# Kernel tuning notes

Hardware: AMD Instinct MI355X
Metric: run time of the kernel (lower is better)

## Reference

```python
import itertools
import jax, jax.numpy as jnp
import numpy as np

B, S, H = 1, 2048, 1024
NH, KVH, HD = 16, 8, 64
E, TOPK, I = 8, 2, 3584
EPS = 1e-6
THETA = 1000000.0
COMBS = np.array(list(itertools.combinations(range(E), TOPK)), dtype=np.int32)  # [28,2]


def setup_inputs() -> dict:
    key = jax.random.key(0)
    ks = jax.random.split(key, 12)
    s = 0.02
    return {
        "hidden_states": jax.random.normal(ks[0], (B, S, H), jnp.float32),
        "ln1_w": jnp.ones((H,), jnp.float32),
        "ln2_w": jnp.ones((H,), jnp.float32),
        "wq": jax.random.normal(ks[1], (NH * HD, H), jnp.float32) * s,
        "wk": jax.random.normal(ks[2], (KVH * HD, H), jnp.float32) * s,
        "wv": jax.random.normal(ks[3], (KVH * HD, H), jnp.float32) * s,
        "wo": jax.random.normal(ks[4], (H, NH * HD), jnp.float32) * s,
        "gate_w": jax.random.normal(ks[5], (E, H), jnp.float32) * s,
        "w1": jax.random.normal(ks[6], (E, I, H), jnp.float32) * s,
        "w2": jax.random.normal(ks[7], (E, H, I), jnp.float32) * s,
        "w3": jax.random.normal(ks[8], (E, I, H), jnp.float32) * s,
    }


def _rmsnorm(x, w):
    v = x.astype(jnp.float32)
    v = v * jax.lax.rsqrt(jnp.mean(v * v, axis=-1, keepdims=True) + EPS)
    return (w * v).astype(x.dtype)


def _rotate_half(x):
    h = x.shape[-1] // 2
    return jnp.concatenate([-x[..., h:], x[..., :h]], axis=-1)


def reference(hidden_states, ln1_w, ln2_w, wq, wk, wv, wo, gate_w, w1, w2, w3):
    residual = hidden_states
    x = _rmsnorm(hidden_states, ln1_w)

    # --- Mixtral attention (GQA + RoPE, causal) ---
    q = (x @ wq.T).reshape(B, S, NH, HD).transpose(0, 2, 1, 3)   # [B,NH,S,HD]
    k = (x @ wk.T).reshape(B, S, KVH, HD).transpose(0, 2, 1, 3)  # [B,KVH,S,HD]
    v = (x @ wv.T).reshape(B, S, KVH, HD).transpose(0, 2, 1, 3)

    pos = jnp.arange(S, dtype=jnp.float32)
    inv_freq = 1.0 / (THETA ** (jnp.arange(0, HD, 2, dtype=jnp.float32) / HD))
    freqs = pos[:, None] * inv_freq[None, :]               # [S,HD/2]
    emb = jnp.concatenate([freqs, freqs], axis=-1)          # [S,HD]
    cos, sin = jnp.cos(emb)[None, None], jnp.sin(emb)[None, None]
    q = q * cos + _rotate_half(q) * sin
    k = k * cos + _rotate_half(k) * sin

    rep = NH // KVH
    k = jnp.repeat(k, rep, axis=1)
    v = jnp.repeat(v, rep, axis=1)

    scores = jnp.einsum("bhsd,bhtd->bhst", q, k) / jnp.sqrt(jnp.float32(HD))
    causal = jnp.tril(jnp.ones((S, S), dtype=bool))
    scores = jnp.where(causal[None, None], scores, jnp.finfo(jnp.float32).min)
    attn = jax.nn.softmax(scores.astype(jnp.float32), axis=-1).astype(q.dtype)
    ctx = jnp.einsum("bhst,bhtd->bhsd", attn, v)
    ctx = ctx.transpose(0, 2, 1, 3).reshape(B, S, NH * HD)
    hidden_states = residual + ctx @ wo.T

    # --- MoE block (combination routing, no experts_used mask) ---
    residual = hidden_states
    x = _rmsnorm(hidden_states, ln2_w).reshape(-1, H)       # [N,H], N=B*S
    N = x.shape[0]
    router_logits = x @ gate_w.T                            # [N,E]
    rw = jax.nn.softmax(router_logits.astype(jnp.float32), axis=-1)

    combs = jnp.asarray(COMBS)                              # [28,2]
    comb_scores = jnp.take(rw, combs, axis=1).sum(-1)       # [N,28]
    sel = jnp.argmax(comb_scores, axis=-1)                  # [N]
    selected_experts = combs[sel]                           # [N,TOPK]
    w = jnp.take_along_axis(rw, selected_experts, axis=1)   # [N,TOPK]
    w = (w / w.sum(-1, keepdims=True)).astype(x.dtype)

    # per-token per-expert combine weights (0 if not selected)
    wm = jnp.zeros((N, E), x.dtype).at[jnp.arange(N)[:, None], selected_experts].set(w)

    # dense evaluation of all experts, combined by sparse weights
    h1 = jax.nn.silu(jnp.einsum("nh,eih->nei", x, w1))
    h3 = jnp.einsum("nh,eih->nei", x, w3)
    out_e = jnp.einsum("nei,ehi->neh", h1 * h3, w2)          # [N,E,H]
    moe_out = jnp.einsum("neh,ne->nh", out_e, wm)

    hidden_states = residual + moe_out.reshape(B, S, H)
    return hidden_states
```

## Files before the change

### kernel.cpp

```cpp
#include <hip/hip_runtime.h>
#include <hip/hip_bf16.h>
#include <math.h>

constexpr int S_ = 2048, H_ = 1024, NH_ = 16, KVH_ = 8, HD_ = 64;
constexpr int E_ = 8, I_ = 3584;
constexpr int KSLC = 4;
constexpr float EPS_ = 1e-6f;
constexpr float THETA_ = 1000000.0f;

#define SDIV(a,b) (((a)+(b)-1)/(b))

typedef __attribute__((ext_vector_type(8))) short bf16x8;
typedef __attribute__((ext_vector_type(4))) float f32x4;

__device__ inline unsigned pkbf(float a, float b) {
    unsigned r;
    asm("v_cvt_pk_bf16_f32 %0, %1, %2" : "=v"(r) : "v"(a), "v"(b));
    return r;
}
__device__ inline unsigned short f2bf(float f) {
    unsigned u = __float_as_uint(f);
    u += 0x7FFF + ((u >> 16) & 1);
    return (unsigned short)(u >> 16);
}
__device__ inline float bf2f(unsigned short v) {
    return __uint_as_float((unsigned)v << 16);
}

__device__ inline void gload16u(const void* gsrc, char* ldsArr, int uoff) {
    int off = __builtin_amdgcn_readfirstlane(uoff);
    __builtin_amdgcn_global_load_lds(
        (__attribute__((address_space(1))) void*)(gsrc),
        (__attribute__((address_space(3))) void*)(ldsArr + off), 16, 0, 0);
}
__device__ inline void vmdrain() {
    asm volatile("s_waitcnt vmcnt(0)" ::: "memory");
}

template<bool WB>
__device__ inline int4 loadW16(const void* W, size_t elemOff) {
    if constexpr (WB) {
        return *(const int4*)((const unsigned short*)W + elemOff);
    } else {
        const float* s = (const float*)W + elemOff;
        float4 f0 = *(const float4*)s, f1 = *(const float4*)(s + 4);
        return make_int4(pkbf(f0.x, f0.y), pkbf(f0.z, f0.w),
                         pkbf(f1.x, f1.y), pkbf(f1.z, f1.w));
    }
}

__global__ __launch_bounds__(256) void conv_bf16(const float* __restrict__ in,
                                                 unsigned short* __restrict__ out, long n8)
{
    long i = (long)blockIdx.x * 256 + threadIdx.x;
    long stride = (long)gridDim.x * 256;
    for (; i < n8; i += stride) {
        const float* s = in + i * 8;
        float4 f0 = *(const float4*)s, f1 = *(const float4*)(s + 4);
        *(int4*)(out + i * 8) = make_int4(pkbf(f0.x, f0.y), pkbf(f0.z, f0.w),
                                          pkbf(f1.x, f1.y), pkbf(f1.z, f1.w));
    }
}

__global__ __launch_bounds__(256) void rmsnorm_k(const float* __restrict__ x,
                                                 const float* __restrict__ w,
                                                 float* __restrict__ out,
                                                 unsigned short* __restrict__ outb)
{
    int row = blockIdx.x;
    int tid = threadIdx.x;
    const float* xr = x + (size_t)row * H_;
    float4 v = *(const float4*)&xr[tid * 4];
    float ss = v.x*v.x + v.y*v.y + v.z*v.z + v.w*v.w;
#pragma unroll
    for (int off = 32; off > 0; off >>= 1) ss += __shfl_xor(ss, off);
    __shared__ float red[4];
    if ((tid & 63) == 0) red[tid >> 6] = ss;
    __syncthreads();
    float tot = red[0] + red[1] + red[2] + red[3];
    float r = rsqrtf(tot / (float)H_ + EPS_);
    float4 wv = *(const float4*)&w[tid * 4];
    float4 o;
    o.x = v.x * r * wv.x; o.y = v.y * r * wv.y;
    o.z = v.z * r * wv.z; o.w = v.w * r * wv.w;
    *(float4*)&out[(size_t)row * H_ + tid * 4] = o;
    if (outb) {
        uint2 pk = make_uint2(pkbf(o.x, o.y), pkbf(o.z, o.w));
        *(uint2*)&outb[(size_t)row * H_ + tid * 4] = pk;
    }
}

template<bool WB>
__global__ __launch_bounds__(256) void dense_mfma(const float* __restrict__ A,
                                                  const void* __restrict__ Bw,
                                                  const float* __restrict__ Res,
                                                  float* __restrict__ C,
                                                  int M, int N, int K)
{
    __shared__ char As[16384], Bs[16384];
    int tid = threadIdx.x;
    int m0 = blockIdx.y * 128, n0 = blockIdx.x * 128;
    int lane = tid & 63, w = tid >> 6, wm = w >> 1, wn = w & 1;
    int lm = lane & 15, lk = lane >> 4;

    int4 rA[4], rB[4];
    auto loadAll = [&](int kb) {
#pragma unroll
        for (int it = 0; it < 4; ++it) {
            int g = tid + it * 256, row = g >> 3, kg = g & 7;
            const float* s = A + (size_t)(m0 + row) * K + kb + kg * 8;
            float4 f0 = *(const float4*)s, f1 = *(const float4*)(s + 4);
            rA[it] = make_int4(pkbf(f0.x, f0.y), pkbf(f0.z, f0.w),
                               pkbf(f1.x, f1.y), pkbf(f1.z, f1.w));
            rB[it] = loadW16<WB>(Bw, (size_t)(n0 + row) * K + kb + kg * 8);
        }
    };
    auto writeAll = [&]() {
#pragma unroll
        for (int it = 0; it < 4; ++it) {
            int g = tid + it * 256, row = g >> 3, kg = g & 7;
            int byte = row * 128 + ((kg * 16) ^ ((row & 7) << 4));
            *(int4*)(As + byte) = rA[it];
            *(int4*)(Bs + byte) = rB[it];
        }
    };

    f32x4 z = {0.f, 0.f, 0.f, 0.f};
    f32x4 acc[4][4];
#pragma unroll
    for (int mf = 0; mf < 4; ++mf)
#pragma unroll
        for (int nf = 0; nf < 4; ++nf) acc[mf][nf] = z;

    loadAll(0);
    for (int kt = 0; kt < K / 64; ++kt) {
        __syncthreads();
        writeAll();
        __syncthreads();
        if (kt + 1 < K / 64) loadAll((kt + 1) * 64);
#pragma unroll
        for (int ks = 0; ks < 2; ++ks) {
            bf16x8 af[4];
#pragma unroll
            for (int mf = 0; mf < 4; ++mf) {
                int row = wm * 64 + mf * 16 + lm;
                af[mf] = *(const bf16x8*)(As + row * 128 + ((ks * 64 + lk * 16) ^ ((row & 7) << 4)));
            }
#pragma unroll
            for (int nf = 0; nf < 4; ++nf) {
                int brow = wn * 64 + nf * 16 + lm;
                bf16x8 bf = *(const bf16x8*)(Bs + brow * 128 + ((ks * 64 + lk * 16) ^ ((brow & 7) << 4)));
#pragma unroll
                for (int mf = 0; mf < 4; ++mf)
                    acc[mf][nf] = __builtin_amdgcn_mfma_f32_16x16x32_bf16(af[mf], bf, acc[mf][nf], 0, 0, 0);
            }
        }
    }

#pragma unroll
    for (int mf = 0; mf < 4; ++mf)
#pragma unroll
        for (int nf = 0; nf < 4; ++nf) {
            int col = n0 + wn * 64 + nf * 16 + lm;
#pragma unroll
            for (int j = 0; j < 4; ++j) {
                int row = m0 + wm * 64 + mf * 16 + lk * 4 + j;
                float r = Res ? Res[(size_t)row * N + col] : 0.0f;
                C[(size_t)row * N + col] = acc[mf][nf][j] + r;
            }
        }
}

__global__ __launch_bounds__(256) void rope_conv(const float* __restrict__ q,
                                                 const float* __restrict__ k,
                                                 unsigned short* __restrict__ qbf,
                                                 unsigned short* __restrict__ kbf)
{
    int idx = blockIdx.x * 256 + threadIdx.x;
    const int totq = S_ * NH_ * 32;
    const int tot = totq + S_ * KVH_ * 32;
    if (idx >= tot) return;
    const float* base; unsigned short* obase; int s, di; float sc;
    if (idx < totq) {
        s = idx / (NH_ * 32); int r = idx % (NH_ * 32);
        size_t o = ((size_t)s * NH_ + (r >> 5)) * HD_;
        base = q + o; obase = qbf + o; di = r & 31; sc = 0.125f;
    } else {
        int j2 = idx - totq;
        s = j2 / (KVH_ * 32); int r = j2 % (KVH_ * 32);
        size_t o = ((size_t)s * KVH_ + (r >> 5)) * HD_;
        base = k + o; obase = kbf + o; di = r & 31; sc = 1.0f;
    }
    float invf = powf(THETA_, -(2.0f * di) / (float)HD_);
    float ang = (float)s * invf;
    float c = cosf(ang), sn = sinf(ang);
    float x0 = base[di], x1 = base[di + 32];
    obase[di]      = f2bf((x0 * c - x1 * sn) * sc);
    obase[di + 32] = f2bf((x1 * c + x0 * sn) * sc);
}

__global__ __launch_bounds__(256) void v_trans(const float* __restrict__ v,
                                               unsigned short* __restrict__ vtb)
{
    int t0 = blockIdx.x * 64, kvh = blockIdx.y;
    __shared__ unsigned short T[64][64];
    int tid = threadIdx.x;
    int k = tid >> 2, d0 = (tid & 3) * 16;
    const float* src = v + ((size_t)(t0 + k) * KVH_ + kvh) * HD_ + d0;
#pragma unroll
    for (int x = 0; x < 4; ++x) {
        float4 f = *(const float4*)(src + x * 4);
        T[k][d0 + x*4 + 0] = f2bf(f.x);
        T[k][d0 + x*4 + 1] = f2bf(f.y);
        T[k][d0 + x*4 + 2] = f2bf(f.z);
        T[k][d0 + x*4 + 3] = f2bf(f.w);
    }
    __syncthreads();
    int d = tid >> 2, s0 = (tid & 3) * 16;
    unsigned short tmp[16] __attribute__((aligned(16)));
#pragma unroll
    for (int x = 0; x < 16; ++x) {
        int s = s0 + x;
        int key = 16 * (s & 3) + (s >> 2);
        tmp[x] = T[key][d];
    }
    unsigned short* dst = vtb + ((size_t)kvh * HD_ + d) * S_ + t0 + s0;
    *(int4*)(dst)     = *(int4*)(tmp);
    *(int4*)(dst + 8) = *(int4*)(tmp + 8);
}

__global__ __launch_bounds__(256) void attn_mfma(const unsigned short* __restrict__ qbf,
                                                 const unsigned short* __restrict__ kbf,
                                                 const unsigned short* __restrict__ vtb,
                                                 float* __restrict__ ctx)
{
    __shared__ char Ps[4 * 2048];
    int pair = blockIdx.x, h = blockIdx.y, z = blockIdx.z;
    int qb = z ? (31 - pair) : pair;
    int q0 = qb * 64;
    int kvh = h >> 1;
    int tid = threadIdx.x;
    int w = tid >> 6, lane = tid & 63;
    int lm = lane & 15, lk = lane >> 4;
    char* myP = Ps + w * 2048;

    bf16x8 qf[2];
    const unsigned short* qrow = qbf + ((size_t)(q0 + w * 16 + lm) * NH_ + h) * HD_;
#pragma unroll
    for (int ks = 0; ks < 2; ++ks)
        qf[ks] = *(const bf16x8*)(qrow + ks * 32 + lk * 8);

    float m_[4], l_[4];
    f32x4 o_[4];
#pragma unroll
    for (int j = 0; j < 4; ++j) { m_[j] = -1e30f; l_[j] = 0.f; }
    f32x4 zf = {0.f, 0.f, 0.f, 0.f};
#pragma unroll
    for (int nd = 0; nd < 4; ++nd) o_[nd] = zf;

    for (int t0 = 0; t0 <= q0; t0 += 64) {
        f32x4 s[4];
#pragma unroll
        for (int nf = 0; nf < 4; ++nf) {
            const unsigned short* krow = kbf + ((size_t)(t0 + nf * 16 + lm) * KVH_ + kvh) * HD_;
            bf16x8 k0 = *(const bf16x8*)(krow + lk * 8);
            bf16x8 k1 = *(const bf16x8*)(krow + 32 + lk * 8);
            f32x4 acc = zf;
            acc = __builtin_amdgcn_mfma_f32_16x16x32_bf16(qf[0], k0, acc, 0, 0, 0);
            acc = __builtin_amdgcn_mfma_f32_16x16x32_bf16(qf[1], k1, acc, 0, 0, 0);
            s[nf] = acc;
        }
        if (t0 == q0) {
#pragma unroll
            for (int nf = 0; nf < 4; ++nf)
#pragma unroll
                for (int j = 0; j < 4; ++j) {
                    int key = nf * 16 + lm, qq = w * 16 + lk * 4 + j;
                    if (key > qq) s[nf][j] = -1e30f;
                }
        }
        float p_[4][4];
#pragma unroll
        for (int j = 0; j < 4; ++j) {
            float mx = fmaxf(fmaxf(s[0][j], s[1][j]), fmaxf(s[2][j], s[3][j]));
#pragma unroll
            for (int off = 8; off > 0; off >>= 1) mx = fmaxf(mx, __shfl_xor(mx, off));
            float nm = fmaxf(m_[j], mx);
            float rs = __expf(m_[j] - nm);
            float sum = 0.f;
#pragma unroll
            for (int nf = 0; nf < 4; ++nf) {
                float pv = __expf(s[nf][j] - nm);
                p_[nf][j] = pv; sum += pv;
            }
#pragma unroll
            for (int off = 8; off > 0; off >>= 1) sum += __shfl_xor(sum, off);
            l_[j] = l_[j] * rs + sum;
            m_[j] = nm;
#pragma unroll
            for (int nd = 0; nd < 4; ++nd) o_[nd][j] *= rs;
        }
#pragma unroll
        for (int j = 0; j < 4; ++j) {
            int r = lk * 4 + j;
            unsigned lo = pkbf(p_[0][j], p_[1][j]);
            unsigned hi = pkbf(p_[2][j], p_[3][j]);
            int byte = (lm * 8) ^ ((r & 7) << 4);
            *(uint2*)(myP + r * 128 + byte) = make_uint2(lo, hi);
        }
#pragma unroll
        for (int ks = 0; ks < 2; ++ks) {
            int byte = (ks * 64 + lk * 16) ^ ((lm & 7) << 4);
            bf16x8 pA = *(const bf16x8*)(myP + lm * 128 + byte);
#pragma unroll
            for (int nd = 0; nd < 4; ++nd) {
                const unsigned short* vrow = vtb + ((size_t)kvh * HD_ + nd * 16 + lm) * S_ + t0 + ks * 32 + lk * 8;
                bf16x8 vB = *(const bf16x8*)vrow;
                o_[nd] = __builtin_amdgcn_mfma_f32_16x16x32_bf16(pA, vB, o_[nd], 0, 0, 0);
            }
        }
    }
#pragma unroll
    for (int nd = 0; nd < 4; ++nd)
#pragma unroll
        for (int j = 0; j < 4; ++j) {
            int r = lk * 4 + j;
            ctx[((size_t)(q0 + w * 16 + r) * NH_ + h) * HD_ + nd * 16 + lm] = o_[nd][j] / l_[j];
        }
}

__global__ __launch_bounds__(64) void router_k(const float* __restrict__ x2,
                                               const float* __restrict__ gw,
                                               int* __restrict__ cnt,
                                               int* __restrict__ elist,
                                               int* __restrict__ eslot,
                                               float* __restrict__ wslot)
{
    int n = blockIdx.x, lane = threadIdx.x;
    float part[E_];
#pragma unroll
    for (int e = 0; e < E_; ++e) part[e] = 0.f;
    const float* xr = x2 + (size_t)n * H_;
    for (int j = lane; j < H_; j += 64) {
        float xv = xr[j];
#pragma unroll
        for (int e = 0; e < E_; ++e) part[e] = fmaf(xv, gw[e * H_ + j], part[e]);
    }
#pragma unroll
    for (int e = 0; e < E_; ++e)
#pragma unroll
        for (int off = 32; off > 0; off >>= 1) part[e] += __shfl_xor(part[e], off);
    if (lane == 0) {
        float mx = part[0];
#pragma unroll
        for (int e = 1; e < E_; ++e) mx = fmaxf(mx, part[e]);
        float rw[E_]; float ssum = 0.f;
#pragma unroll
        for (int e = 0; e < E_; ++e) { rw[e] = expf(part[e] - mx); ssum += rw[e]; }
#pragma unroll
        for (int e = 0; e < E_; ++e) rw[e] /= ssum;
        float best = -1.f; int ba = 0, bb = 1;
        for (int a = 0; a < E_; ++a)
            for (int b = a + 1; b < E_; ++b) {
                float scv = rw[a] + rw[b];
                if (scv > best) { best = scv; ba = a; bb = b; }
            }
        float wa = rw[ba], wb = rw[bb], wsum = wa + wb;
        wa /= wsum; wb /= wsum;
        int p = atomicAdd(&cnt[ba], 1);
        elist[ba * S_ + p] = n; eslot[ba * S_ + p] = 2 * n;
        p = atomicAdd(&cnt[bb], 1);
        elist[bb * S_ + p] = n; eslot[bb * S_ + p] = 2 * n + 1;
        wslot[2 * n] = wa; wslot[2 * n + 1] = wb;
    }
}

__global__ __launch_bounds__(256) void moe_up_g(const unsigned short* __restrict__ x2b,
                                                const unsigned short* __restrict__ w1b,
                                                const unsigned short* __restrict__ w3b,
                                                const int* __restrict__ cnt,
                                                const int* __restrict__ elist,
                                                const int* __restrict__ eslot,
                                                unsigned short* __restrict__ hbuf)
{
    int e = blockIdx.z;
    int c = cnt[e];
    int p0 = blockIdx.y * 128;
    if (p0 >= c) return;
    int i0 = blockIdx.x * 64;
    int tid = threadIdx.x;

    __shared__ char As[16384], B1s[8192], B3s[8192];
    __shared__ int rowtokS[128], rowslotS[128];
    if (tid < 128) {
        int p = min(p0 + tid, c - 1);
        rowtokS[tid]  = elist[e * S_ + p];
        rowslotS[tid] = eslot[e * S_ + p];
    }
    __syncthreads();

    int lane = tid & 63, w = tid >> 6, wm = w >> 1, wn = w & 1;
    int lm = lane & 15, lk = lane >> 4;
    int wb16 = (tid & ~63) * 16;
    size_t wbase = (size_t)e * I_ * H_;

    f32x4 z = {0.f, 0.f, 0.f, 0.f};
    f32x4 acc1[4][2], acc3[4][2];
#pragma unroll
    for (int mf = 0; mf < 4; ++mf)
#pragma unroll
        for (int nf = 0; nf < 2; ++nf) { acc1[mf][nf] = z; acc3[mf][nf] = z; }

    for (int kt = 0; kt < H_ / 64; ++kt) {
        int kb = kt * 64;
#pragma unroll
        for (int it = 0; it < 4; ++it) {
            int g = tid + it * 256, row = g >> 3, kg = g & 7;
            int kgs = kg ^ (row & 7);
            gload16u(x2b + (size_t)rowtokS[row] * H_ + kb + kgs * 8, As, wb16 + it * 4096);
        }
#pragma unroll
        for (int it = 0; it < 2; ++it) {
            int g = tid + it * 256, row = g >> 3, kg = g & 7;
            int kgs = kg ^ (row & 7);
            size_t off = wbase + (size_t)(i0 + row) * H_ + kb + kgs * 8;
            gload16u(w1b + off, B1s, wb16 + it * 4096);
            gload16u(w3b + off, B3s, wb16 + it * 4096);
        }
        vmdrain();
        __syncthreads();
#pragma unroll
        for (int ks = 0; ks < 2; ++ks) {
            bf16x8 af[4];
#pragma unroll
            for (int mf = 0; mf < 4; ++mf) {
                int row = wm * 64 + mf * 16 + lm;
                af[mf] = *(const bf16x8*)(As + row * 128 + ((ks * 64 + lk * 16) ^ ((row & 7) << 4)));
            }
#pragma unroll
            for (int nf = 0; nf < 2; ++nf) {
                int brow = wn * 32 + nf * 16 + lm;
                int bby = brow * 128 + ((ks * 64 + lk * 16) ^ ((brow & 7) << 4));
                bf16x8 b1 = *(const bf16x8*)(B1s + bby);
                bf16x8 b3 = *(const bf16x8*)(B3s + bby);
#pragma unroll
                for (int mf = 0; mf < 4; ++mf) {
                    acc1[mf][nf] = __builtin_amdgcn_mfma_f32_16x16x32_bf16(af[mf], b1, acc1[mf][nf], 0, 0, 0);
                    acc3[mf][nf] = __builtin_amdgcn_mfma_f32_16x16x32_bf16(af[mf], b3, acc3[mf][nf], 0, 0, 0);
                }
            }
        }
        __syncthreads();
    }

#pragma unroll
    for (int mf = 0; mf < 4; ++mf)
#pragma unroll
        for (int nf = 0; nf < 2; ++nf) {
            int coli = i0 + wn * 32 + nf * 16 + lm;
#pragma unroll
            for (int j = 0; j < 4; ++j) {
                int rloc = wm * 64 + mf * 16 + lk * 4 + j;
                if (p0 + rloc < c) {
                    float h1 = acc1[mf][nf][j];
                    float val = h1 / (1.f + __expf(-h1)) * acc3[mf][nf][j];
                    hbuf[(size_t)rowslotS[rloc] * I_ + coli] = f2bf(val);
                }
            }
        }
}

__global__ __launch_bounds__(256) void moe_dn_g(const unsigned short* __restrict__ hbuf,
                                                const unsigned short* __restrict__ w2b,
                                                const int* __restrict__ cnt,
                                                const int* __restrict__ eslot,
                                                unsigned short* __restrict__ dbuf)
{
    int e = blockIdx.z >> 2;
    int slice = blockIdx.z & 3;
    int c = cnt[e];
    int p0 = blockIdx.y * 128;
    if (p0 >= c) return;
    int h0 = blockIdx.x * 128;
    int tid = threadIdx.x;
    const int kb0 = slice * (I_ / KSLC);

    __shared__ char As[16384], Bs[16384];
    __shared__ int rowslotS[128];
    if (tid < 128) rowslotS[tid] = eslot[e * S_ + min(p0 + tid, c - 1)];
    __syncthreads();

    int lane = tid & 63, w = tid >> 6, wm = w >> 1, wn = w & 1;
    int lm = lane & 15, lk = lane >> 4;
    int wb16 = (tid & ~63) * 16;
    size_t wbase = (size_t)e * H_ * I_;

    f32x4 z = {0.f, 0.f, 0.f, 0.f};
    f32x4 acc[4][4];
#pragma unroll
    for (int mf = 0; mf < 4; ++mf)
#pragma unroll
        for (int nf = 0; nf < 4; ++nf) acc[mf][nf] = z;

    const int NKT = (I_ / KSLC) / 64;
    for (int kt = 0; kt < NKT; ++kt) {
        int kb = kb0 + kt * 64;
#pragma unroll
        for (int it = 0; it < 4; ++it) {
            int g = tid + it * 256, row = g >> 3, kg = g & 7;
            int kgs = kg ^ (row & 7);
            gload16u(hbuf + (size_t)rowslotS[row] * I_ + kb + kgs * 8, As, wb16 + it * 4096);
            gload16u(w2b + wbase + (size_t)(h0 + row) * I_ + kb + kgs * 8, Bs, wb16 + it * 4096);
        }
        vmdrain();
        __syncthreads();
#pragma unroll
        for (int ks = 0; ks < 2; ++ks) {
            bf16x8 af[4];
#pragma unroll
            for (int mf = 0; mf < 4; ++mf) {
                int row = wm * 64 + mf * 16 + lm;
                af[mf] = *(const bf16x8*)(As + row * 128 + ((ks * 64 + lk * 16) ^ ((row & 7) << 4)));
            }
#pragma unroll
            for (int nf = 0; nf < 4; ++nf) {
                int brow = wn * 64 + nf * 16 + lm;
                bf16x8 bf = *(const bf16x8*)(Bs + brow * 128 + ((ks * 64 + lk * 16) ^ ((brow & 7) << 4)));
#pragma unroll
                for (int mf = 0; mf < 4; ++mf)
                    acc[mf][nf] = __builtin_amdgcn_mfma_f32_16x16x32_bf16(af[mf], bf, acc[mf][nf], 0, 0, 0);
            }
        }
        __syncthreads();
    }

    unsigned short* dslice = dbuf + (size_t)slice * S_ * 2 * H_;
#pragma unroll
    for (int mf = 0; mf < 4; ++mf)
#pragma unroll
        for (int nf = 0; nf < 4; ++nf) {
            int colh = h0 + wn * 64 + nf * 16 + lm;
#pragma unroll
            for (int j = 0; j < 4; ++j) {
                int rloc = wm * 64 + mf * 16 + lk * 4 + j;
                if (p0 + rloc < c)
                    dslice[(size_t)rowslotS[rloc] * H_ + colh] = f2bf(acc[mf][nf][j]);
            }
        }
}

template<bool WB>
__global__ __launch_bounds__(256) void moe_up_mfma(const float* __restrict__ x2,
                                                   const void* __restrict__ w1,
                                                   const void* __restrict__ w3,
                                                   const int* __restrict__ cnt,
                                                   const int* __restrict__ elist,
                                                   const int* __restrict__ eslot,
                                                   unsigned short* __restrict__ hbuf)
{
    int e = blockIdx.z;
    int c = cnt[e];
    int p0 = blockIdx.y * 128;
    if (p0 >= c) return;
    int i0 = blockIdx.x * 64;
    int tid = threadIdx.x;

    __shared__ char As[16384], B1s[8192], B3s[8192];
    __shared__ int rowtokS[128], rowslotS[128];
    if (tid < 128) {
        int p = min(p0 + tid, c - 1);
        rowtokS[tid]  = elist[e * S_ + p];
        rowslotS[tid] = eslot[e * S_ + p];
    }
    __syncthreads();

    int lane = tid & 63, w = tid >> 6, wm = w >> 1, wn = w & 1;
    int lm = lane & 15, lk = lane >> 4;
    size_t wbase = (size_t)e * I_ * H_;

    int4 rA[4], rB1[2], rB3[2];
    auto loadAll = [&](int kb) {
#pragma unroll
        for (int it = 0; it < 4; ++it) {
            int g = tid + it * 256, row = g >> 3, kg = g & 7;
            const float* s = x2 + (size_t)rowtokS[row] * H_ + kb + kg * 8;
            float4 f0 = *(const float4*)s, f1 = *(const float4*)(s + 4);
            rA[it] = make_int4(pkbf(f0.x, f0.y), pkbf(f0.z, f0.w),
                               pkbf(f1.x, f1.y), pkbf(f1.z, f1.w));
        }
#pragma unroll
        for (int it = 0; it < 2; ++it) {
            int g = tid + it * 256, row = g >> 3, kg = g & 7;
            size_t off = wbase + (size_t)(i0 + row) * H_ + kb + kg * 8;
            rB1[it] = loadW16<WB>(w1, off);
            rB3[it] = loadW16<WB>(w3, off);
        }
    };
    auto writeAll = [&]() {
#pragma unroll
        for (int it = 0; it < 4; ++it) {
            int g = tid + it * 256, row = g >> 3, kg = g & 7;
            int byte = row * 128 + ((kg * 16) ^ ((row & 7) << 4));
            *(int4*)(As + byte) = rA[it];
        }
#pragma unroll
        for (int it = 0; it < 2; ++it) {
            int g = tid + it * 256, row = g >> 3, kg = g & 7;
            int byte = row * 128 + ((kg * 16) ^ ((row & 7) << 4));
            *(int4*)(B1s + byte) = rB1[it];
            *(int4*)(B3s + byte) = rB3[it];
        }
    };

    f32x4 z = {0.f, 0.f, 0.f, 0.f};
    f32x4 acc1[4][2], acc3[4][2];
#pragma unroll
    for (int mf = 0; mf < 4; ++mf)
#pragma unroll
        for (int nf = 0; nf < 2; ++nf) { acc1[mf][nf] = z; acc3[mf][nf] = z; }

    loadAll(0);
    for (int kt = 0; kt < H_ / 64; ++kt) {
        __syncthreads();
        writeAll();
        __syncthreads();
        if (kt + 1 < H_ / 64) loadAll((kt + 1) * 64);
#pragma unroll
        for (int ks = 0; ks < 2; ++ks) {
            bf16x8 af[4];
#pragma unroll
            for (int mf = 0; mf < 4; ++mf) {
                int row = wm * 64 + mf * 16 + lm;
                af[mf] = *(const bf16x8*)(As + row * 128 + ((ks * 64 + lk * 16) ^ ((row & 7) << 4)));
            }
#pragma unroll
            for (int nf = 0; nf < 2; ++nf) {
                int brow = wn * 32 + nf * 16 + lm;
                int bby = brow * 128 + ((ks * 64 + lk * 16) ^ ((brow & 7) << 4));
                bf16x8 b1 = *(const bf16x8*)(B1s + bby);
                bf16x8 b3 = *(const bf16x8*)(B3s + bby);
#pragma unroll
                for (int mf = 0; mf < 4; ++mf) {
                    acc1[mf][nf] = __builtin_amdgcn_mfma_f32_16x16x32_bf16(af[mf], b1, acc1[mf][nf], 0, 0, 0);
                    acc3[mf][nf] = __builtin_amdgcn_mfma_f32_16x16x32_bf16(af[mf], b3, acc3[mf][nf], 0, 0, 0);
                }
            }
        }
    }

#pragma unroll
    for (int mf = 0; mf < 4; ++mf)
#pragma unroll
        for (int nf = 0; nf < 2; ++nf) {
            int coli = i0 + wn * 32 + nf * 16 + lm;
#pragma unroll
            for (int j = 0; j < 4; ++j) {
                int rloc = wm * 64 + mf * 16 + lk * 4 + j;
                if (p0 + rloc < c) {
                    float h1 = acc1[mf][nf][j];
                    float val = h1 / (1.f + __expf(-h1)) * acc3[mf][nf][j];
                    hbuf[(size_t)rowslotS[rloc] * I_ + coli] = f2bf(val);
                }
            }
        }
}

template<bool WB>
__global__ __launch_bounds__(256) void moe_dn_mfma(const unsigned short* __restrict__ hbuf,
                                                   const void* __restrict__ w2,
                                                   const int* __restrict__ cnt,
                                                   const int* __restrict__ eslot,
                                                   unsigned short* __restrict__ dbuf)
{
    int e = blockIdx.z >> 2;
    int slice = blockIdx.z & 3;
    int c = cnt[e];
    int p0 = blockIdx.y * 128;
    if (p0 >= c) return;
    int h0 = blockIdx.x * 128;
    int tid = threadIdx.x;
    const int kb0 = slice * (I_ / KSLC);

    __shared__ char As[16384], Bs[16384];
    __shared__ int rowslotS[128];
    if (tid < 128) rowslotS[tid] = eslot[e * S_ + min(p0 + tid, c - 1)];
    __syncthreads();

    int lane = tid & 63, w = tid >> 6, wm = w >> 1, wn = w & 1;
    int lm = lane & 15, lk = lane >> 4;
    size_t wbase = (size_t)e * H_ * I_;

    int4 rA[4], rB[4];
    auto loadAll = [&](int kb) {
#pragma unroll
        for (int it = 0; it < 4; ++it) {
            int g = tid + it * 256, row = g >> 3, kg = g & 7;
            rA[it] = *(const int4*)(hbuf + (size_t)rowslotS[row] * I_ + kb + kg * 8);
            rB[it] = loadW16<WB>(w2, wbase + (size_t)(h0 + row) * I_ + kb + kg * 8);
        }
    };
    auto writeAll = [&]() {
#pragma unroll
        for (int it = 0; it < 4; ++it) {
            int g = tid + it * 256, row = g >> 3, kg = g & 7;
            int byte = row * 128 + ((kg * 16) ^ ((row & 7) << 4));
            *(int4*)(As + byte) = rA[it];
            *(int4*)(Bs + byte) = rB[it];
        }
    };

    f32x4 z = {0.f, 0.f, 0.f, 0.f};
    f32x4 acc[4][4];
#pragma unroll
    for (int mf = 0; mf < 4; ++mf)
#pragma unroll
        for (int nf = 0; nf < 4; ++nf) acc[mf][nf] = z;

    loadAll(kb0);
    const int NKT = (I_ / KSLC) / 64;
    for (int kt = 0; kt < NKT; ++kt) {
        __syncthreads();
        writeAll();
        __syncthreads();
        if (kt + 1 < NKT) loadAll(kb0 + (kt + 1) * 64);
#pragma unroll
        for (int ks = 0; ks < 2; ++ks) {
            bf16x8 af[4];
#pragma unroll
            for (int mf = 0; mf < 4; ++mf) {
                int row = wm * 64 + mf * 16 + lm;
                af[mf] = *(const bf16x8*)(As + row * 128 + ((ks * 64 + lk * 16) ^ ((row & 7) << 4)));
            }
#pragma unroll
            for (int nf = 0; nf < 4; ++nf) {
                int brow = wn * 64 + nf * 16 + lm;
                bf16x8 bf = *(const bf16x8*)(Bs + brow * 128 + ((ks * 64 + lk * 16) ^ ((brow & 7) << 4)));
#pragma unroll
                for (int mf = 0; mf < 4; ++mf)
                    acc[mf][nf] = __builtin_amdgcn_mfma_f32_16x16x32_bf16(af[mf], bf, acc[mf][nf], 0, 0, 0);
            }
        }
    }

    unsigned short* dslice = dbuf + (size_t)slice * S_ * 2 * H_;
#pragma unroll
    for (int mf = 0; mf < 4; ++mf)
#pragma unroll
        for (int nf = 0; nf < 4; ++nf) {
            int colh = h0 + wn * 64 + nf * 16 + lm;
#pragma unroll
            for (int j = 0; j < 4; ++j) {
                int rloc = wm * 64 + mf * 16 + lk * 4 + j;
                if (p0 + rloc < c)
                    dslice[(size_t)rowslotS[rloc] * H_ + colh] = f2bf(acc[mf][nf][j]);
            }
        }
}

__global__ __launch_bounds__(256) void combine_k(const float* __restrict__ hid2,
                                                 const unsigned short* __restrict__ dbuf,
                                                 const float* __restrict__ wslot,
                                                 float* __restrict__ out)
{
    int idx = blockIdx.x * 256 + threadIdx.x;
    if (idx >= S_ * H_) return;
    int n = idx >> 10;
    int hcol = idx & (H_ - 1);
    float s0 = 0.f, s1 = 0.f;
#pragma unroll
    for (int sl = 0; sl < KSLC; ++sl) {
        const unsigned short* base = dbuf + (size_t)sl * S_ * 2 * H_;
        s0 += bf2f(base[(size_t)(2 * n)     * H_ + hcol]);
        s1 += bf2f(base[(size_t)(2 * n + 1) * H_ + hcol]);
    }
    out[idx] = hid2[idx] + wslot[2 * n] * s0 + wslot[2 * n + 1] * s1;
}

extern "C" void kernel_launch(void* const* d_in, const int* in_sizes, int n_in,
                              void* d_out, int out_size, void* d_ws, size_t ws_size,
                              hipStream_t stream)
{
    const float* hidden = (const float*)d_in[0];
    const float* ln1    = (const float*)d_in[1];
    const float* ln2    = (const float*)d_in[2];
    const float* wq     = (const float*)d_in[3];
    const float* wk     = (const float*)d_in[4];
    const float* wv     = (const float*)d_in[5];
    const float* wo     = (const float*)d_in[6];
    const float* gw     = (const float*)d_in[7];
    const float* w1     = (const float*)d_in[8];
    const float* w2     = (const float*)d_in[9];
    const float* w3     = (const float*)d_in[10];
    float* out = (float*)d_out;

    char* p = (char*)d_ws;
    auto alignp = [&]() { p = (char*)(((uintptr_t)p + 255) & ~(uintptr_t)255); };
    auto alloc_f = [&](size_t n) { alignp(); float* r = (float*)p; p += n * 4; return r; };
    auto alloc_h = [&](size_t n) { alignp(); unsigned short* r = (unsigned short*)p; p += n * 2; return r; };
    auto alloc_i = [&](size_t n) { alignp(); int* r = (int*)p; p += n * 4; return r; };

    float* xb   = alloc_f((size_t)S_ * H_);
    float* q    = alloc_f((size_t)S_ * NH_ * HD_);
    float* kb   = alloc_f((size_t)S_ * KVH_ * HD_);
    float* vb   = alloc_f((size_t)S_ * KVH_ * HD_);
    float* hid2 = alloc_f((size_t)S_ * H_);
    float* x2   = alloc_f((size_t)S_ * H_);
    unsigned short* x2b  = alloc_h((size_t)S_ * H_);
    unsigned short* hbuf = alloc_h((size_t)S_ * 2 * I_);
    unsigned short* dbuf = alloc_h((size_t)KSLC * S_ * 2 * H_);
    float* wslot= alloc_f((size_t)S_ * 2);
    unsigned short* qbf = alloc_h((size_t)S_ * NH_ * HD_);
    unsigned short* kbf = alloc_h((size_t)S_ * KVH_ * HD_);
    unsigned short* vtb = alloc_h((size_t)KVH_ * HD_ * S_);
    int* cnt   = alloc_i(E_);
    int* elist = alloc_i((size_t)E_ * S_);
    int* eslot = alloc_i((size_t)E_ * S_);
    float* ctx = xb;

    size_t used = (size_t)(p - (char*)d_ws);
    const size_t nW = (size_t)E_ * I_ * H_;
    size_t wbf_bytes = (3 * nW + (size_t)(NH_*HD_ + 2*KVH_*HD_ + H_) * H_) * 2 + 4096;
    bool WB = ws_size > used && (ws_size - used) >= wbf_bytes;

    unsigned short *w1b = nullptr, *w3b = nullptr, *w2b = nullptr;
    unsigned short *wqb = nullptr, *wkb = nullptr, *wvb = nullptr, *wob = nullptr;
    if (WB) {
        w1b = alloc_h(nW); w3b = alloc_h(nW); w2b = alloc_h(nW);
        wqb = alloc_h((size_t)NH_ * HD_ * H_);
        wkb = alloc_h((size_t)KVH_ * HD_ * H_);
        wvb = alloc_h((size_t)KVH_ * HD_ * H_);
        wob = alloc_h((size_t)H_ * NH_ * HD_);
    }

    hipMemsetAsync(cnt, 0, E_ * sizeof(int), stream);

    if (WB) {
        conv_bf16<<<2048, 256, 0, stream>>>(w1, w1b, (long)(nW / 8));
        conv_bf16<<<2048, 256, 0, stream>>>(w3, w3b, (long)(nW / 8));
        conv_bf16<<<2048, 256, 0, stream>>>(w2, w2b, (long)(nW / 8));
        conv_bf16<<<512, 256, 0, stream>>>(wq, wqb, (long)((size_t)NH_*HD_*H_ / 8));
        conv_bf16<<<512, 256, 0, stream>>>(wk, wkb, (long)((size_t)KVH_*HD_*H_ / 8));
        conv_bf16<<<512, 256, 0, stream>>>(wv, wvb, (long)((size_t)KVH_*HD_*H_ / 8));
        conv_bf16<<<512, 256, 0, stream>>>(wo, wob, (long)((size_t)H_*NH_*HD_ / 8));
    }

    rmsnorm_k<<<S_, 256, 0, stream>>>(hidden, ln1, xb, nullptr);

    if (WB) {
        dense_mfma<true><<<dim3(8, 16),  256, 0, stream>>>(xb, wqb, nullptr, q,  S_, NH_ * HD_, H_);
        dense_mfma<true><<<dim3(4, 16),  256, 0, stream>>>(xb, wkb, nullptr, kb, S_, KVH_ * HD_, H_);
        dense_mfma<true><<<dim3(4, 16),  256, 0, stream>>>(xb, wvb, nullptr, vb, S_, KVH_ * HD_, H_);
    } else {
        dense_mfma<false><<<dim3(8, 16), 256, 0, stream>>>(xb, wq, nullptr, q,  S_, NH_ * HD_, H_);
        dense_mfma<false><<<dim3(4, 16), 256, 0, stream>>>(xb, wk, nullptr, kb, S_, KVH_ * HD_, H_);
        dense_mfma<false><<<dim3(4, 16), 256, 0, stream>>>(xb, wv, nullptr, vb, S_, KVH_ * HD_, H_);
    }
    {
        int tot = S_ * (NH_ + KVH_) * 32;
        rope_conv<<<SDIV(tot, 256), 256, 0, stream>>>(q, kb, qbf, kbf);
    }
    v_trans<<<dim3(S_ / 64, KVH_), 256, 0, stream>>>(vb, vtb);
    attn_mfma<<<dim3(16, NH_, 2), 256, 0, stream>>>(qbf, kbf, vtb, ctx);

    if (WB)
        dense_mfma<true><<<dim3(8, 16),  256, 0, stream>>>(ctx, wob, hidden, hid2, S_, H_, NH_ * HD_);
    else
        dense_mfma<false><<<dim3(8, 16), 256, 0, stream>>>(ctx, wo, hidden, hid2, S_, H_, NH_ * HD_);

    rmsnorm_k<<<S_, 256, 0, stream>>>(hid2, ln2, x2, x2b);
    router_k<<<S_, 64, 0, stream>>>(x2, gw, cnt, elist, eslot, wslot);

    if (WB) {
        moe_up_g<<<dim3(I_ / 64, S_ / 128, E_), 256, 0, stream>>>(x2b, w1b, w3b, cnt, elist, eslot, hbuf);
        moe_dn_g<<<dim3(H_ / 128, S_ / 128, E_ * KSLC), 256, 0, stream>>>(hbuf, w2b, cnt, eslot, dbuf);
    } else {
        moe_up_mfma<false><<<dim3(I_ / 64, S_ / 128, E_), 256, 0, stream>>>(x2, w1, w3, cnt, elist, eslot, hbuf);
        moe_dn_mfma<false><<<dim3(H_ / 128, S_ / 128, E_ * KSLC), 256, 0, stream>>>(hbuf, w2, cnt, eslot, dbuf);
    }
    combine_k<<<SDIV(S_ * H_, 256), 256, 0, stream>>>(hid2, dbuf, wslot, out);
}
```

Baseline: 539.1 us.

## Fuse QKV projections into one bf16 GEMM with bf16 activations

Concatenates the Q, K and V weights into one bf16 matrix and runs a single bf16-input GEMM (new dense_g kernel, 128x64 tiles, 512 blocks) that writes bf16 QKV output. RoPE and V-transpose kernels now read that bf16 buffer, and attention also writes a bf16 context copy that feeds the output projection through the same bf16 GEMM. This removes fp32 activation loads and conversions and two kernel launches, and gives more blocks per GEMM for better occupancy. In exchange attention writes an extra bf16 context buffer, and q/k are rounded to bf16 before RoPE, which may add small numerical error.

```diff
diff --git a/kernel.cpp b/kernel.cpp
--- a/kernel.cpp
+++ b/kernel.cpp
@@ -90,6 +90,82 @@
     }
 }
 
+template<bool OUTF32>
+__global__ __launch_bounds__(256) void dense_g(const unsigned short* __restrict__ A,
+                                               const unsigned short* __restrict__ B,
+                                               const float* __restrict__ Res,
+                                               void* __restrict__ C,
+                                               int K, int ldC)
+{
+    int m0 = blockIdx.y * 128, n0 = blockIdx.x * 64;
+    int tid = threadIdx.x;
+    __shared__ char As[16384], Bs[8192];
+    int lane = tid & 63, w = tid >> 6, wm = w >> 1, wn = w & 1;
+    int lm = lane & 15, lk = lane >> 4;
+    int wb16 = (tid & ~63) * 16;
+
+    f32x4 z = {0.f, 0.f, 0.f, 0.f};
+    f32x4 acc[4][2];
+#pragma unroll
+    for (int mf = 0; mf < 4; ++mf)
+#pragma unroll
+        for (int nf = 0; nf < 2; ++nf) acc[mf][nf] = z;
+
+    for (int kt = 0; kt < K / 64; ++kt) {
+        int kb = kt * 64;
+#pragma unroll
+        for (int it = 0; it < 4; ++it) {
+            int g = tid + it * 256, row = g >> 3, kg = g & 7;
+            int kgs = kg ^ (row & 7);
+            gload16u(A + (size_t)(m0 + row) * K + kb + kgs * 8, As, wb16 + it * 4096);
+        }
+#pragma unroll
+        for (int it = 0; it < 2; ++it) {
+            int g = tid + it * 256, row = g >> 3, kg = g & 7;
+            int kgs = kg ^ (row & 7);
+            gload16u(B + (size_t)(n0 + row) * K + kb + kgs * 8, Bs, wb16 + it * 4096);
+        }
+        vmdrain();
+        __syncthreads();
+#pragma unroll
+        for (int ks = 0; ks < 2; ++ks) {
+            bf16x8 af[4];
+#pragma unroll
+            for (int mf = 0; mf < 4; ++mf) {
+                int row = wm * 64 + mf * 16 + lm;
+                af[mf] = *(const bf16x8*)(As + row * 128 + ((ks * 64 + lk * 16) ^ ((row & 7) << 4)));
+            }
+#pragma unroll
+            for (int nf = 0; nf < 2; ++nf) {
+                int brow = wn * 32 + nf * 16 + lm;
+                bf16x8 bf = *(const bf16x8*)(Bs + brow * 128 + ((ks * 64 + lk * 16) ^ ((brow & 7) << 4)));
+#pragma unroll
+                for (int mf = 0; mf < 4; ++mf)
+                    acc[mf][nf] = __builtin_amdgcn_mfma_f32_16x16x32_bf16(af[mf], bf, acc[mf][nf], 0, 0, 0);
+            }
+        }
+        __syncthreads();
+    }
+
+#pragma unroll
+    for (int mf = 0; mf < 4; ++mf)
+#pragma unroll
+        for (int nf = 0; nf < 2; ++nf) {
+            int col = n0 + wn * 32 + nf * 16 + lm;
+#pragma unroll
+            for (int j = 0; j < 4; ++j) {
+                int row = m0 + wm * 64 + mf * 16 + lk * 4 + j;
+                float v = acc[mf][nf][j];
+                if constexpr (OUTF32) {
+                    float r = Res ? Res[(size_t)row * ldC + col] : 0.0f;
+                    ((float*)C)[(size_t)row * ldC + col] = v + r;
+                } else {
+                    ((unsigned short*)C)[(size_t)row * ldC + col] = f2bf(v);
+                }
+            }
+        }
+}
+
 template<bool WB>
 __global__ __launch_bounds__(256) void dense_mfma(const float* __restrict__ A,
                                                   const void* __restrict__ Bw,
@@ -169,6 +245,59 @@
                 C[(size_t)row * N + col] = acc[mf][nf][j] + r;
             }
         }
+}
+
+__global__ __launch_bounds__(256) void rope_conv_b(const unsigned short* __restrict__ qkvb,
+                                                   unsigned short* __restrict__ qbf,
+                                                   unsigned short* __restrict__ kbf)
+{
+    int idx = blockIdx.x * 256 + threadIdx.x;
+    const int totq = S_ * NH_ * 32;
+    const int tot = totq + S_ * KVH_ * 32;
+    if (idx >= tot) return;
+    const unsigned short* src; unsigned short* dst; int s, di; float sc;
+    if (idx < totq) {
+        s = idx / (NH_ * 32); int r = idx % (NH_ * 32); int h = r >> 5;
+        src = qkvb + (size_t)s * 2048 + h * 64;
+        dst = qbf + ((size_t)s * NH_ + h) * HD_;
+        di = r & 31; sc = 0.125f;
+    } else {
+        int j2 = idx - totq;
+        s = j2 / (KVH_ * 32); int r = j2 % (KVH_ * 32); int kvh = r >> 5;
+        src = qkvb + (size_t)s * 2048 + 1024 + kvh * 64;
+        dst = kbf + ((size_t)s * KVH_ + kvh) * HD_;
+        di = r & 31; sc = 1.0f;
+    }
+    float invf = powf(THETA_, -(2.0f * di) / (float)HD_);
+    float ang = (float)s * invf;
+    float c = cosf(ang), sn = sinf(ang);
+    float x0 = bf2f(src[di]), x1 = bf2f(src[di + 32]);
+    dst[di]      = f2bf((x0 * c - x1 * sn) * sc);
+    dst[di + 32] = f2bf((x1 * c + x0 * sn) * sc);
+}
+
+__global__ __launch_bounds__(256) void v_trans_b(const unsigned short* __restrict__ qkvb,
+                                                 unsigned short* __restrict__ vtb)
+{
+    int t0 = blockIdx.x * 64, kvh = blockIdx.y;
+    __shared__ unsigned short T[64][64];
+    int tid = threadIdx.x;
+    int k = tid >> 2, d0 = (tid & 3) * 16;
+    const unsigned short* src = qkvb + (size_t)(t0 + k) * 2048 + 1536 + kvh * 64 + d0;
+    *(int4*)&T[k][d0]     = *(const int4*)(src);
+    *(int4*)&T[k][d0 + 8] = *(const int4*)(src + 8);
+    __syncthreads();
+    int d = tid >> 2, s0 = (tid & 3) * 16;
+    unsigned short tmp[16] __attribute__((aligned(16)));
+#pragma unroll
+    for (int x = 0; x < 16; ++x) {
+        int s = s0 + x;
+        int key = 16 * (s & 3) + (s >> 2);
+        tmp[x] = T[key][d];
+    }
+    unsigned short* dst = vtb + ((size_t)kvh * HD_ + d) * S_ + t0 + s0;
+    *(int4*)(dst)     = *(int4*)(tmp);
+    *(int4*)(dst + 8) = *(int4*)(tmp + 8);
 }
 
 __global__ __launch_bounds__(256) void rope_conv(const float* __restrict__ q,
@@ -232,7 +361,8 @@
 __global__ __launch_bounds__(256) void attn_mfma(const unsigned short* __restrict__ qbf,
                                                  const unsigned short* __restrict__ kbf,
                                                  const unsigned short* __restrict__ vtb,
-                                                 float* __restrict__ ctx)
+                                                 float* __restrict__ ctx,
+                                                 unsigned short* __restrict__ ctxb)
 {
     __shared__ char Ps[4 * 2048];
     int pair = blockIdx.x, h = blockIdx.y, z = blockIdx.z;
@@ -325,7 +455,10 @@
 #pragma unroll
         for (int j = 0; j < 4; ++j) {
             int r = lk * 4 + j;
-            ctx[((size_t)(q0 + w * 16 + r) * NH_ + h) * HD_ + nd * 16 + lm] = o_[nd][j] / l_[j];
+            float val = o_[nd][j] / l_[j];
+            size_t oidx = ((size_t)(q0 + w * 16 + r) * NH_ + h) * HD_ + nd * 16 + lm;
+            ctx[oidx] = val;
+            ctxb[oidx] = f2bf(val);
         }
 }
 
@@ -800,12 +933,15 @@
     auto alloc_i = [&](size_t n) { alignp(); int* r = (int*)p; p += n * 4; return r; };
 
     float* xb   = alloc_f((size_t)S_ * H_);
+    unsigned short* xbb = alloc_h((size_t)S_ * H_);
     float* q    = alloc_f((size_t)S_ * NH_ * HD_);
     float* kb   = alloc_f((size_t)S_ * KVH_ * HD_);
     float* vb   = alloc_f((size_t)S_ * KVH_ * HD_);
+    unsigned short* qkvb = alloc_h((size_t)S_ * 2048);
     float* hid2 = alloc_f((size_t)S_ * H_);
     float* x2   = alloc_f((size_t)S_ * H_);
     unsigned short* x2b  = alloc_h((size_t)S_ * H_);
+    unsigned short* ctxb = alloc_h((size_t)S_ * H_);
     unsigned short* hbuf = alloc_h((size_t)S_ * 2 * I_);
     unsigned short* dbuf = alloc_h((size_t)KSLC * S_ * 2 * H_);
     float* wslot= alloc_f((size_t)S_ * 2);
@@ -819,16 +955,14 @@
 
     size_t used = (size_t)(p - (char*)d_ws);
     const size_t nW = (size_t)E_ * I_ * H_;
-    size_t wbf_bytes = (3 * nW + (size_t)(NH_*HD_ + 2*KVH_*HD_ + H_) * H_) * 2 + 4096;
+    size_t wbf_bytes = (3 * nW + (size_t)2048 * H_ + (size_t)H_ * NH_ * HD_) * 2 + 8192;
     bool WB = ws_size > used && (ws_size - used) >= wbf_bytes;
 
     unsigned short *w1b = nullptr, *w3b = nullptr, *w2b = nullptr;
-    unsigned short *wqb = nullptr, *wkb = nullptr, *wvb = nullptr, *wob = nullptr;
+    unsigned short *wqkvb = nullptr, *wob = nullptr;
     if (WB) {
         w1b = alloc_h(nW); w3b = alloc_h(nW); w2b = alloc_h(nW);
-        wqb = alloc_h((size_t)NH_ * HD_ * H_);
-        wkb = alloc_h((size_t)KVH_ * HD_ * H_);
-        wvb = alloc_h((size_t)KVH_ * HD_ * H_);
+        wqkvb = alloc_h((size_t)2048 * H_);
         wob = alloc_h((size_t)H_ * NH_ * HD_);
     }
 
@@ -838,34 +972,35 @@
         conv_bf16<<<2048, 256, 0, stream>>>(w1, w1b, (long)(nW / 8));
         conv_bf16<<<2048, 256, 0, stream>>>(w3, w3b, (long)(nW / 8));
         conv_bf16<<<2048, 256, 0, stream>>>(w2, w2b, (long)(nW / 8));
-        conv_bf16<<<512, 256, 0, stream>>>(wq, wqb, (long)((size_t)NH_*HD_*H_ / 8));
-        conv_bf16<<<512, 256, 0, stream>>>(wk, wkb, (long)((size_t)KVH_*HD_*H_ / 8));
-        conv_bf16<<<512, 256, 0, stream>>>(wv, wvb, (long)((size_t)KVH_*HD_*H_ / 8));
+        conv_bf16<<<512, 256, 0, stream>>>(wq, wqkvb, (long)((size_t)NH_*HD_*H_ / 8));
+        conv_bf16<<<256, 256, 0, stream>>>(wk, wqkvb + (size_t)NH_*HD_*H_, (long)((size_t)KVH_*HD_*H_ / 8));
+        conv_bf16<<<256, 256, 0, stream>>>(wv, wqkvb + (size_t)(NH_+KVH_)*HD_*H_, (long)((size_t)KVH_*HD_*H_ / 8));
         conv_bf16<<<512, 256, 0, stream>>>(wo, wob, (long)((size_t)H_*NH_*HD_ / 8));
     }
 
-    rmsnorm_k<<<S_, 256, 0, stream>>>(hidden, ln1, xb, nullptr);
+    rmsnorm_k<<<S_, 256, 0, stream>>>(hidden, ln1, xb, WB ? xbb : nullptr);
 
     if (WB) {
-        dense_mfma<true><<<dim3(8, 16),  256, 0, stream>>>(xb, wqb, nullptr, q,  S_, NH_ * HD_, H_);
-        dense_mfma<true><<<dim3(4, 16),  256, 0, stream>>>(xb, wkb, nullptr, kb, S_, KVH_ * HD_, H_);
-        dense_mfma<true><<<dim3(4, 16),  256, 0, stream>>>(xb, wvb, nullptr, vb, S_, KVH_ * HD_, H_);
+        dense_g<false><<<dim3(32, 16), 256, 0, stream>>>(xbb, wqkvb, nullptr, qkvb, H_, 2048);
+        {
+            int tot = S_ * (NH_ + KVH_) * 32;
+            rope_conv_b<<<SDIV(tot, 256), 256, 0, stream>>>(qkvb, qbf, kbf);
+        }
+        v_trans_b<<<dim3(S_ / 64, KVH_), 256, 0, stream>>>(qkvb, vtb);
+        attn_mfma<<<dim3(16, NH_, 2), 256, 0, stream>>>(qbf, kbf, vtb, ctx, ctxb);
+        dense_g<true><<<dim3(16, 16), 256, 0, stream>>>(ctxb, wob, hidden, hid2, H_, H_);
     } else {
         dense_mfma<false><<<dim3(8, 16), 256, 0, stream>>>(xb, wq, nullptr, q,  S_, NH_ * HD_, H_);
         dense_mfma<false><<<dim3(4, 16), 256, 0, stream>>>(xb, wk, nullptr, kb, S_, KVH_ * HD_, H_);
         dense_mfma<false><<<dim3(4, 16), 256, 0, stream>>>(xb, wv, nullptr, vb, S_, KVH_ * HD_, H_);
-    }
-    {
-        int tot = S_ * (NH_ + KVH_) * 32;
-        rope_conv<<<SDIV(tot, 256), 256, 0, stream>>>(q, kb, qbf, kbf);
-    }
-    v_trans<<<dim3(S_ / 64, KVH_), 256, 0, stream>>>(vb, vtb);
-    attn_mfma<<<dim3(16, NH_, 2), 256, 0, stream>>>(qbf, kbf, vtb, ctx);
-
-    if (WB)
-        dense_mfma<true><<<dim3(8, 16),  256, 0, stream>>>(ctx, wob, hidden, hid2, S_, H_, NH_ * HD_);
-    else
+        {
+            int tot = S_ * (NH_ + KVH_) * 32;
+            rope_conv<<<SDIV(tot, 256), 256, 0, stream>>>(q, kb, qbf, kbf);
+        }
+        v_trans<<<dim3(S_ / 64, KVH_), 256, 0, stream>>>(vb, vtb);
+        attn_mfma<<<dim3(16, NH_, 2), 256, 0, stream>>>(qbf, kbf, vtb, ctx, ctxb);
         dense_mfma<false><<<dim3(8, 16), 256, 0, stream>>>(ctx, wo, hidden, hid2, S_, H_, NH_ * HD_);
+    }
 
     rmsnorm_k<<<S_, 256, 0, stream>>>(hid2, ln2, x2, x2b);
     router_k<<<S_, 64, 0, stream>>>(x2, gw, cnt, elist, eslot, wslot);
```

After: 467.5 us. 13.3% less time.
